# Kernel tuning notes

Measured on AMD Instinct MI355X. Metric: run time of the kernel, lower is better.

## Reference

```python
import math
import jax, jax.numpy as jnp
import numpy as np

B, NH, T, N, D = 4, 8, 2048, 256, 512
THETA = 2 ** 16
LN_EPS = 1e-5
RETRIEVAL_SCALE = 1.0
TWO_PI = 2.0 * math.pi


def _freqs(n):
    # get_freqs: 1/theta**(floor(i/2)*2 / n) / (2*pi)
    i = jnp.arange(n, dtype=jnp.float32)
    q = jnp.floor(i / 2.0) * 2.0
    return 1.0 / (THETA ** (q / n)) / TWO_PI


def _rope(phases, v):
    # phases: [1,1,T,N]; v: [B,nh,T,N]
    ph = (phases % 1.0) * TWO_PI
    pc, ps = jnp.cos(ph), jnp.sin(ph)
    ve, vo = v[..., ::2], v[..., 1::2]
    v_rot = jnp.stack((-vo, ve), axis=-1).reshape(v.shape)  # interleaved rotate
    return v * pc + v_rot * ps


def _l2norm(x):
    return x / jnp.maximum(jnp.linalg.norm(x, axis=-1, keepdims=True), 1e-12)


def setup_inputs() -> dict:
    key = jax.random.key(0)
    ks = jax.random.split(key, 8)
    return {
        "Q": jax.random.normal(ks[0], (B, NH, T, N), jnp.float32),
        "V": jax.random.normal(ks[1], (B, NH, T, D), jnp.float32),
        "x_raw": jax.random.normal(ks[2], (B, T, D), jnp.float32),
        "x_next": jax.random.normal(ks[3], (B, T, D), jnp.float32),
        "theta_Q_w": 0.02 * jax.random.normal(ks[4], (N, D), jnp.float32),
        "theta_K_w": 0.02 * jax.random.normal(ks[5], (N, D), jnp.float32),
        "beta_w": 0.02 * jax.random.normal(ks[6], (NH, D), jnp.float32),
        "memory_gate": jnp.full((1, NH, 1, 1), -2.0, jnp.float32),
        "M0": 0.02 * jax.random.normal(ks[7], (B, NH, N, D), jnp.float32),
    }


def _forward(Q, V, x_raw, x_next, theta_Q_w, theta_K_w, beta_w, memory_gate, M0):
    Bq, nh, Tq, Nq = Q.shape
    # ---- causal RoPE linear attention (K is Q; strictly lower-triangular, no softmax)
    freqs = _freqs(Nq)  # [N]
    phases = jnp.arange(Tq, dtype=jnp.float32)[None, None, :, None] * freqs[None, None, None, :]
    QR = _rope(phases, Q)
    scores = jnp.einsum('bhtn,bhsn->bhts', QR, QR)
    mask = jnp.tril(jnp.ones((Tq, Tq), bool), -1)  # diagonal=-1
    scores = jnp.where(mask, scores, 0.0)
    y_standard = scores @ V  # [B,nh,T,D]

    # ---- memory retrieval (position-invariant query)
    Qm = _l2norm(x_raw @ theta_Q_w.T)  # [B,T,N], shared across heads
    y_memory = jnp.einsum('btn,bhnd->bhtd', Qm, M0)
    mu = y_memory.mean(-1, keepdims=True)
    var = y_memory.var(-1, keepdims=True)  # biased, like torch LayerNorm
    y_memory = (y_memory - mu) * jax.lax.rsqrt(var + LN_EPS) * RETRIEVAL_SCALE

    # ---- delta-rule memory update (detached in the original)
    Km = _l2norm(jax.lax.stop_gradient(x_raw @ theta_K_w.T))         # [B,T,N]
    beta = jax.nn.sigmoid(jax.lax.stop_gradient(x_raw @ beta_w.T))   # [B,T,nh]
    Vm = jax.lax.stop_gradient(x_next)                               # [B,T,D]
    M_init = jax.lax.stop_gradient(M0)

    def step(M, inp):
        k, v, b = inp  # k:[B,N] shared across heads, v:[B,D], b:[B,nh]
        v_old = jnp.einsum('bn,bhnd->bhd', k, M)
        v_new = b[..., None] * v[:, None, :] + (1.0 - b[..., None]) * v_old
        M = M + jnp.einsum('bn,bhd->bhnd', k, v_new - v_old)
        return M, None

    M_new, _ = jax.lax.scan(
        step, M_init,
        (jnp.swapaxes(Km, 0, 1), jnp.swapaxes(Vm, 0, 1), jnp.swapaxes(beta, 0, 1)))

    gate = jax.nn.sigmoid(memory_gate)  # [1,nh,1,1]
    y = (1.0 - gate) * y_standard + gate * y_memory
    return y, M_new


def reference(Q, V, x_raw, x_next, theta_Q_w, theta_K_w, beta_w, memory_gate, M0):
    return _forward(Q, V, x_raw, x_next, theta_Q_w, theta_K_w, beta_w, memory_gate, M0)
```

## Files before the change

kernel.cpp:

```cpp
#include <hip/hip_runtime.h>
#include <hip/hip_bf16.h>
#include <math.h>

#define BBATCH 4
#define NHEAD  8
#define TSEQ   2048
#define NDIM   256
#define DDIM   512

typedef float f32x4 __attribute__((ext_vector_type(4)));
typedef short bf16x8 __attribute__((ext_vector_type(8)));

typedef __attribute__((address_space(3))) unsigned int lds_uint;
typedef __attribute__((address_space(1))) unsigned int g_uint;

__device__ __forceinline__ unsigned short f2bf(float f) {
  __hip_bfloat16 h = __float2bfloat16(f);
  return *reinterpret_cast<unsigned short*>(&h);
}
__device__ __forceinline__ float bf2f(unsigned short u) {
  __hip_bfloat16 h;
  *reinterpret_cast<unsigned short*>(&h) = u;
  return __bfloat162float(h);
}
// ... 235 lines not shown
    int koff = (ks * 32 + khi * 8) * 2;
    bf16x8 ah = *(const bf16x8*)((const char*)Khi + arow * 512 + (koff ^ ((arow & 7) << 4)));
    bf16x8 al = *(const bf16x8*)((const char*)Klo + arow * 512 + (koff ^ ((arow & 7) << 4)));
    bf16x8 bhf[4], blf[4];
#pragma unroll
    for (int si = 0; si < 4; ++si) {
      int brow = si * 16 + l16;
      bhf[si] = *(const bf16x8*)((const char*)Khi + brow * 512 + (koff ^ ((brow & 7) << 4)));
      blf[si] = *(const bf16x8*)((const char*)Klo + brow * 512 + (koff ^ ((brow & 7) << 4)));
    }
#pragma unroll
    for (int si = 0; si < 4; ++si) sacc[si] = mfma16(ah, bhf[si], sacc[si]);
#pragma unroll
    for (int si = 0; si < 4; ++si) sacc[si] = mfma16(ah, blf[si], sacc[si]);
#pragma unroll
    for (int si = 0; si < 4; ++si) sacc[si] = mfma16(al, bhf[si], sacc[si]);
  }
#pragma unroll
  for (int si = 0; si < 4; ++si)
#pragma unroll
    for (int r = 0; r < 4; ++r) {
      int t = wave * 16 + khi * 4 + r, s = si * 16 + l16;
      Bm[t * 64 + s] = (s < t) ? bv[t] * sacc[si][r] : 0.f;
    }
  __syncthreads();
  if (wave == 0) {
    float x[64];
#pragma unroll
    for (int i = 0; i < 64; ++i) x[i] = 0.f;
    long base = (long)blk * 4096;
    const f32x4* BmV = (const f32x4*)Bm;
    float bl = bv[lane];
#pragma unroll
    for (int t = 0; t < 64; ++t) {
      float p0 = 0.f, p1 = 0.f, p2 = 0.f, p3 = 0.f;
#pragma unroll
      for (int rq = 0; rq < 16; ++rq) {
        f32x4 b4 = BmV[t * 16 + rq];
        p0 = fmaf(b4.x, x[rq * 4 + 0], p0);
        p1 = fmaf(b4.y, x[rq * 4 + 1], p1);
        p2 = fmaf(b4.z, x[rq * 4 + 2], p2);
        p3 = fmaf(b4.w, x[rq * 4 + 3], p3);
      }
      float xv = ((lane == t) ? 1.f : 0.f) - ((p0 + p1) + (p2 + p3));
      x[t] = xv;
      float wv = xv * bl;
      unsigned short hi = f2bf(wv);
      Whi[base + t * 64 + lane] = hi;
      Wlo[base + t * 64 + lane] = f2bf(wv - bf2f(hi));
    }
  }
}

__global__ __launch_bounds__(256) void cscan_kernel(
    const unsigned short* __restrict__ Kb,
    const unsigned short* __restrict__ KbT,
    const float* __restrict__ xn,
    const float* __restrict__ M0,
    const unsigned short* __restrict__ Whi,
    const unsigned short* __restrict__ Wlo,
    float* __restrict__ Mout) {
  __shared__ unsigned short Mthi[64 * 256];
  __shared__ unsigned short Mtlo[64 * 256];
  __shared__ unsigned short Kr[64 * 256];
  __shared__ unsigned short Pool[16384];
  __shared__ unsigned short RU0[64 * 64];
  __shared__ unsigned short RU1[64 * 64];
  unsigned short* Wh = Pool;
  unsigned short* Wl = Pool + 4096;
  unsigned short* Krt = Pool;
  int bh = blockIdx.x, dsl = blockIdx.y;
  int b = bh >> 3;
  int d0 = dsl * 64;
  int tid = threadIdx.x, wave = tid >> 6, lane = tid & 63;
  int khi = lane >> 4, l16 = lane & 15;
  const char* KbBase = (const char*)(Kb + (long)b * TSEQ * 256);

  f32x4 macc[4][4];
  const float* M0p = M0 + (long)bh * 256 * 512;
#pragma unroll
  for (int ni = 0; ni < 4; ++ni)
#pragma unroll
    for (int di = 0; di < 4; ++di)
#pragma unroll
      for (int r = 0; r < 4; ++r) {
        int n = wave * 64 + ni * 16 + khi * 4 + r;
        macc[ni][di][r] = M0p[(long)n * 512 + d0 + di * 16 + l16];
      }
#pragma unroll
  for (int ni = 0; ni < 4; ++ni)
#pragma unroll
    for (int di = 0; di < 4; ++di) {
      int n = wave * 64 + ni * 16 + khi * 4;
      int d = di * 16 + l16;
      unsigned short hq[4], lq[4];
#pragma unroll
      for (int r = 0; r < 4; ++r) {
        float v = macc[ni][di][r];
        hq[r] = f2bf(v); lq[r] = f2bf(v - bf2f(hq[r]));
      }
      int off = d * 512 + (((n * 2) ^ ((d & 7) << 4)));
      *(uint2*)((char*)Mthi + off) =
          make_uint2((unsigned)hq[0] | ((unsigned)hq[1] << 16),
                     (unsigned)hq[2] | ((unsigned)hq[3] << 16));
      *(uint2*)((char*)Mtlo + off) =
          make_uint2((unsigned)lq[0] | ((unsigned)lq[1] << 16),
                     (unsigned)lq[2] | ((unsigned)lq[3] << 16));
    }
#pragma unroll
  for (int q = 0; q < 8; ++q) {
    int lin = tid * 16 + q * 4096;
    int t = lin >> 9;
    int c = (lin & 511) ^ KSW(t);
    __builtin_amdgcn_global_load_lds((const g_uint*)(KbBase + (long)t * 512 + c),
                                     (lds_uint*)((char*)Kr + lin), 16, 0, 0);
  }
  __syncthreads();

  for (int ch = 0; ch < 32; ++ch) {
    int tc0 = ch * 64;
    {
      const char* whb = (const char*)(Whi + ((long)bh * 32 + ch) * 4096);
      const char* wlb = (const char*)(Wlo + ((long)bh * 32 + ch) * 4096);
#pragma unroll
      for (int q = 0; q < 2; ++q) {
        int lin = tid * 16 + q * 4096;
        int t = lin >> 7, c = lin & 127;
        int sb = t * 128 + (c ^ ((t & 7) << 4));
        __builtin_amdgcn_global_load_lds((const g_uint*)(whb + sb),
                                         (lds_uint*)((char*)Wh + lin), 16, 0, 0);
        __builtin_amdgcn_global_load_lds((const g_uint*)(wlb + sb),
                                         (lds_uint*)((char*)Wl + lin), 16, 0, 0);
      }
    }
    float vreg[4][4];
    {
      const float* vp = xn + ((long)b * TSEQ + tc0) * 512 + d0;
#pragma unroll
      for (int di = 0; di < 4; ++di)
#pragma unroll
        for (int r = 0; r < 4; ++r) {
          int t = wave * 16 + khi * 4 + r;
          vreg[di][r] = vp[(long)t * 512 + di * 16 + l16];
        }
    }
    __syncthreads();

    f32x4 aacc[4] = {};
#pragma unroll
    for (int ks = 0; ks < 8; ++ks) {
      int arow = wave * 16 + l16;
      int koff = (ks * 32 + khi * 8) * 2;
      bf16x8 af = *(const bf16x8*)((const char*)Kr + arow * 512 + (koff ^ KSW(arow)));
      bf16x8 mh[4], ml[4];
#pragma unroll
      for (int di = 0; di < 4; ++di) {
        int drow = di * 16 + l16;
        mh[di] = *(const bf16x8*)((const char*)Mthi + drow * 512 + (koff ^ ((drow & 7) << 4)));
        ml[di] = *(const bf16x8*)((const char*)Mtlo + drow * 512 + (koff ^ ((drow & 7) << 4)));
      }
#pragma unroll
      for (int di = 0; di < 4; ++di) aacc[di] = mfma16(af, mh[di], aacc[di]);
#pragma unroll
      for (int di = 0; di < 4; ++di) aacc[di] = mfma16(af, ml[di], aacc[di]);
    }
#pragma unroll
    for (int di = 0; di < 4; ++di) {
      int t = wave * 16 + khi * 4;
      int d = di * 16 + l16;
      unsigned short rq[4];
#pragma unroll
      for (int r = 0; r < 4; ++r) rq[r] = f2bf(vreg[di][r] - aacc[di][r]);
      int off = d * 128 + (((t * 2) ^ ((d & 7) << 4)));
      *(uint2*)((char*)RU0 + off) =
          make_uint2((unsigned)rq[0] | ((unsigned)rq[1] << 16),
                     (unsigned)rq[2] | ((unsigned)rq[3] << 16));
    }
    __syncthreads();

    if (ch + 1 < 32) {
      const char* kb2 = KbBase + (long)(tc0 + 64) * 512;
#pragma unroll
      for (int q = 0; q < 8; ++q) {
        int lin = tid * 16 + q * 4096;
        int t = lin >> 9;
        int c = (lin & 511) ^ KSW(t);
        __builtin_amdgcn_global_load_lds((const g_uint*)(kb2 + (long)t * 512 + c),
                                         (lds_uint*)((char*)Kr + lin), 16, 0, 0);
      }
    }

    f32x4 uacc[4] = {};
#pragma unroll
    for (int ks = 0; ks < 2; ++ks) {
      int arow = wave * 16 + l16;
      int soff = (ks * 32 + khi * 8) * 2;
      bf16x8 wh_ = *(const bf16x8*)((const char*)Wh + arow * 128 + (soff ^ ((arow & 7) << 4)));
      bf16x8 wl_ = *(const bf16x8*)((const char*)Wl + arow * 128 + (soff ^ ((arow & 7) << 4)));
      bf16x8 rf[4];
#pragma unroll
      for (int di = 0; di < 4; ++di) {
        int drow = di * 16 + l16;
        rf[di] = *(const bf16x8*)((const char*)RU0 + drow * 128 + (soff ^ ((drow & 7) << 4)));
      }
#pragma unroll
      for (int di = 0; di < 4; ++di) uacc[di] = mfma16(wh_, rf[di], uacc[di]);
#pragma unroll
      for (int di = 0; di < 4; ++di) uacc[di] = mfma16(wl_, rf[di], uacc[di]);
    }
    __syncthreads();

    {
#pragma unroll
      for (int q = 0; q < 8; ++q) {
        int lin = tid * 16 + q * 4096;
        int n = lin >> 7, c = lin & 127;
        long sb = ((long)(b * 256 + n)) * 4096 + (long)tc0 * 2 + (c ^ ((n & 7) << 4));
        __builtin_amdgcn_global_load_lds((const g_uint*)((const char*)KbT + sb),
                                         (lds_uint*)((char*)Krt + lin), 16, 0, 0);
      }
    }
#pragma unroll
    for (int di = 0; di < 4; ++di) {
      int t = wave * 16 + khi * 4;
      int d = di * 16 + l16;
      unsigned short hq[4], lq[4];
#pragma unroll
      for (int r = 0; r < 4; ++r) {
        float u = uacc[di][r];
        hq[r] = f2bf(u); lq[r] = f2bf(u - bf2f(hq[r]));
      }
      int off = d * 128 + (((t * 2) ^ ((d & 7) << 4)));
      *(uint2*)((char*)RU0 + off) =
          make_uint2((unsigned)hq[0] | ((unsigned)hq[1] << 16),
                     (unsigned)hq[2] | ((unsigned)hq[3] << 16));
      *(uint2*)((char*)RU1 + off) =
          make_uint2((unsigned)lq[0] | ((unsigned)lq[1] << 16),
                     (unsigned)lq[2] | ((unsigned)lq[3] << 16));
    }
    __syncthreads();

#pragma unroll
    for (int ks = 0; ks < 2; ++ks) {
      int toff = (ks * 32 + khi * 8) * 2;
      bf16x8 ka[4];
#pragma unroll
      for (int ni = 0; ni < 4; ++ni) {
        int n = wave * 64 + ni * 16 + l16;
        ka[ni] = *(const bf16x8*)((const char*)Krt + n * 128 + (toff ^ ((n & 7) << 4)));
      }
      bf16x8 uh[4], ul[4];
#pragma unroll
      for (int di = 0; di < 4; ++di) {
        int drow = di * 16 + l16;
        uh[di] = *(const bf16x8*)((const char*)RU0 + drow * 128 + (toff ^ ((drow & 7) << 4)));
        ul[di] = *(const bf16x8*)((const char*)RU1 + drow * 128 + (toff ^ ((drow & 7) << 4)));
      }
#pragma unroll
      for (int ni = 0; ni < 4; ++ni)
#pragma unroll
        for (int di = 0; di < 4; ++di)
          macc[ni][di] = mfma16(ka[ni], uh[di], macc[ni][di]);
#pragma unroll
      for (int ni = 0; ni < 4; ++ni)
#pragma unroll
        for (int di = 0; di < 4; ++di)
          macc[ni][di] = mfma16(ka[ni], ul[di], macc[ni][di]);
    }
#pragma unroll
    for (int ni = 0; ni < 4; ++ni)
#pragma unroll
      for (int di = 0; di < 4; ++di) {
        int n = wave * 64 + ni * 16 + khi * 4;
        int d = di * 16 + l16;
        unsigned short hq[4], lq[4];
#pragma unroll
        for (int r = 0; r < 4; ++r) {
          float v = macc[ni][di][r];
          hq[r] = f2bf(v); lq[r] = f2bf(v - bf2f(hq[r]));
        }
        int off = d * 512 + (((n * 2) ^ ((d & 7) << 4)));
        *(uint2*)((char*)Mthi + off) =
            make_uint2((unsigned)hq[0] | ((unsigned)hq[1] << 16),
                       (unsigned)hq[2] | ((unsigned)hq[3] << 16));
        *(uint2*)((char*)Mtlo + off) =
            make_uint2((unsigned)lq[0] | ((unsigned)lq[1] << 16),
                       (unsigned)lq[2] | ((unsigned)lq[3] << 16));
      }
    __syncthreads();
  }

  float* Mo = Mout + (long)bh * 256 * 512;
#pragma unroll
  for (int ni = 0; ni < 4; ++ni)
#pragma unroll
    for (int di = 0; di < 4; ++di)
#pragma unroll
      for (int r = 0; r < 4; ++r) {
        int n = wave * 64 + ni * 16 + khi * 4 + r;
        Mo[(long)n * 512 + d0 + di * 16 + l16] = macc[ni][di][r];
      }
}

__global__ __launch_bounds__(512) void attn_kernel(
    const unsigned short* __restrict__ QR,
    const unsigned short* __restrict__ Vt,
    float* __restrict__ Y) {
  int bh = blockIdx.x;
  int bp = blockIdx.y;
  int wave = threadIdx.x >> 6, lane = threadIdx.x & 63;
  int wr = wave >> 2, wc = wave & 3;
  int khi = lane >> 4, l16 = lane & 15;
  __shared__ unsigned short K_lds[64 * 256];
  __shared__ unsigned short S_lds[128 * 64];
  const unsigned short* QRb = QR + (long)bh * TSEQ * 256;
  const unsigned short* Vtb = Vt + (long)bh * 512 * TSEQ;
  float* yb = Y + (long)bh * TSEQ * 512;
  int lin_base = wave * 4096 + lane * 16;

#pragma unroll 1
  for (int half = 0; half < 2; ++half) {
    int bt = half ? bp : (15 - bp);
    int t0 = bt * 128;
    int nst = 2 * bt + 2;

    bf16x8 qa[8];
    {
      int trow = t0 + wave * 16 + l16;
      const unsigned short* qp = QRb + (long)trow * 256 + khi * 8;
#pragma unroll
      for (int ks = 0; ks < 8; ++ks) qa[ks] = *(const bf16x8*)(qp + ks * 32);
    }
    f32x4 acc[4][8] = {};

#pragma unroll
    for (int q = 0; q < 4; ++q) {
      int linear = lin_base + q * 1024;
      int row = linear >> 9;
      int nc2 = (linear & 511) ^ ((row & 7) << 4);
      __builtin_amdgcn_global_load_lds(
          (const g_uint*)((const char*)QRb + (long)row * 512 + nc2),
          (lds_uint*)((char*)K_lds + (wave * 4 + q) * 1024), 16, 0, 0);
    }
    __syncthreads();

    for (int st = 0; st < nst; ++st) {
      int s0 = st * 64;
      f32x4 sacc[4] = {};
#pragma unroll
      for (int ks = 0; ks < 8; ++ks) {
#pragma unroll
        for (int fc = 0; fc < 4; ++fc) {
          int srow = fc * 16 + l16;
          bf16x8 kf = *(const bf16x8*)(
              (const char*)K_lds + srow * 512 + ((ks * 64 + khi * 16) ^ ((srow & 7) << 4)));
          sacc[fc] = mfma16(qa[ks], kf, sacc[fc]);
        }
      }
#pragma unroll
      for (int fc = 0; fc < 4; ++fc)
#pragma unroll
        for (int r = 0; r < 4; ++r) {
          int srow = wave * 16 + khi * 4 + r;
          int scol = fc * 16 + l16;
          float v = ((s0 + scol) < (t0 + srow)) ? sacc[fc][r] : 0.f;
          *(unsigned short*)(
              (char*)S_lds + srow * 128 + ((scol * 2) ^ ((srow & 7) << 4))) = f2bf(v);
        }
      __syncthreads();

      if (st + 1 < nst) {
        long srow_base = (long)(s0 + 64) * 512;
#pragma unroll
        for (int q = 0; q < 4; ++q) {
          int linear = lin_base + q * 1024;
          int row = linear >> 9;
          int nc2 = (linear & 511) ^ ((row & 7) << 4);
          __builtin_amdgcn_global_load_lds(
              (const g_uint*)((const char*)QRb + srow_base + (long)row * 512 + nc2),
              (lds_uint*)((char*)K_lds + (wave * 4 + q) * 1024), 16, 0, 0);
        }
      }
#pragma unroll
      for (int k2 = 0; k2 < 2; ++k2) {
        bf16x8 af[4];
#pragma unroll
        for (int mi = 0; mi < 4; ++mi) {
          int row = wr * 64 + mi * 16 + l16;
          af[mi] = *(const bf16x8*)(
              (const char*)S_lds + row * 128 + ((k2 * 64 + khi * 16) ^ ((row & 7) << 4)));
        }
#pragma unroll
        for (int nh = 0; nh < 2; ++nh) {
          bf16x8 bfv[4];
#pragma unroll
          for (int nj = 0; nj < 4; ++nj) {
            int d = wc * 128 + (nh * 4 + nj) * 16 + l16;
            bfv[nj] = *(const bf16x8*)(Vtb + (long)d * TSEQ + s0 + k2 * 32 + khi * 8);
          }
#pragma unroll
          for (int mi = 0; mi < 4; ++mi)
#pragma unroll
            for (int nj = 0; nj < 4; ++nj)
              acc[mi][nh * 4 + nj] = mfma16(af[mi], bfv[nj], acc[mi][nh * 4 + nj]);
        }
      }
      __syncthreads();
    }

#pragma unroll
    for (int mi = 0; mi < 4; ++mi)
#pragma unroll
      for (int ni = 0; ni < 8; ++ni)
#pragma unroll
        for (int r = 0; r < 4; ++r) {
          int trow = t0 + wr * 64 + mi * 16 + khi * 4 + r;
          int d = wc * 128 + ni * 16 + l16;
          yb[(long)trow * 512 + d] = acc[mi][ni][r];
        }
  }
}

__global__ __launch_bounds__(512) void combine_kernel(
    const unsigned short* __restrict__ Qm,
    const unsigned short* __restrict__ M0t,
    const float* __restrict__ mg,
    float* __restrict__ Y) {
  int t0 = blockIdx.x * 64;
  int bh = blockIdx.y;
  int b = bh >> 3, h = bh & 7;
  int wv = threadIdx.x >> 6, lane = threadIdx.x & 63;
  int khi = lane >> 4, l16 = lane & 15;
  __shared__ unsigned short A_lds[64 * 256];
  __shared__ float red_s[8][64], red_q[8][64];
  __shared__ float mu_s[64], inv_s[64];
  {
    const unsigned short* src = Qm + ((long)b * TSEQ + t0) * 256;
#pragma unroll
    for (int p = 0; p < 4; ++p) {
      int row = (threadIdx.x >> 5) + p * 16;
      int nc = (threadIdx.x & 31) * 8;
      bf16x8 v = *reinterpret_cast<const bf16x8*>(src + (long)row * 256 + nc);
      *reinterpret_cast<bf16x8*>((char*)A_lds + row * 512 + ((nc * 2) ^ ((row & 7) << 4))) = v;
    }
  }
  __syncthreads();
  f32x4 acc[4][4] = {};
  const unsigned short* Bp = M0t + (long)bh * 512 * 256;
#pragma unroll
  for (int ks = 0; ks < 8; ++ks) {
    bf16x8 a[4], bfr[4];
#pragma unroll
    for (int mi = 0; mi < 4; ++mi) {
      int row = mi * 16 + l16;
      a[mi] = *reinterpret_cast<const bf16x8*>(
          (const char*)A_lds + row * 512 + ((ks * 64 + khi * 16) ^ ((row & 7) << 4)));
    }
#pragma unroll
    for (int ni = 0; ni < 4; ++ni) {
      int d = wv * 64 + ni * 16 + l16;
      bfr[ni] = *reinterpret_cast<const bf16x8*>(Bp + (long)d * 256 + ks * 32 + khi * 8);
    }
#pragma unroll
    for (int mi = 0; mi < 4; ++mi)
#pragma unroll
      for (int ni = 0; ni < 4; ++ni)
        acc[mi][ni] = mfma16(a[mi], bfr[ni], acc[mi][ni]);
  }
  float ps[4][4], pq[4][4];
#pragma unroll
  for (int mi = 0; mi < 4; ++mi)
#pragma unroll
    for (int r = 0; r < 4; ++r) {
      float s = 0.f, q = 0.f;
#pragma unroll
      for (int ni = 0; ni < 4; ++ni) {
        float v = acc[mi][ni][r];
        s += v; q += v * v;
      }
      ps[mi][r] = s; pq[mi][r] = q;
    }
#pragma unroll
  for (int off = 1; off < 16; off <<= 1)
#pragma unroll
    for (int mi = 0; mi < 4; ++mi)
#pragma unroll
      for (int r = 0; r < 4; ++r) {
        ps[mi][r] += __shfl_xor(ps[mi][r], off);
        pq[mi][r] += __shfl_xor(pq[mi][r], off);
      }
  if (l16 == 0) {
#pragma unroll
    for (int mi = 0; mi < 4; ++mi)
#pragma unroll
      for (int r = 0; r < 4; ++r) {
        int row = mi * 16 + khi * 4 + r;
        red_s[wv][row] = ps[mi][r];
        red_q[wv][row] = pq[mi][r];
      }
  }
  __syncthreads();
  if (threadIdx.x < 64) {
    float s = 0.f, q = 0.f;
#pragma unroll
    for (int w2 = 0; w2 < 8; ++w2) { s += red_s[w2][threadIdx.x]; q += red_q[w2][threadIdx.x]; }
    float mu = s / 512.f;
    float var = q / 512.f - mu * mu;
    mu_s[threadIdx.x] = mu;
    inv_s[threadIdx.x] = rsqrtf(var + 1e-5f);
  }
  __syncthreads();
  float gate = 1.f / (1.f + expf(-mg[h]));
  float omg = 1.f - gate;
  float* yb = Y + ((long)bh * TSEQ + t0) * 512;
#pragma unroll
  for (int mi = 0; mi < 4; ++mi)
#pragma unroll
    for (int r = 0; r < 4; ++r) {
      int row = mi * 16 + khi * 4 + r;
      float mu = mu_s[row], inv = inv_s[row];
#pragma unroll
      for (int ni = 0; ni < 4; ++ni) {
        int d = wv * 64 + ni * 16 + l16;
        long off = (long)row * 512 + d;
        float ymv = (acc[mi][ni][r] - mu) * inv;
        yb[off] = omg * yb[off] + gate * ymv;
      }
    }
}

extern "C" void kernel_launch(void* const* d_in, const int* in_sizes, int n_in,
                              void* d_out, int out_size, void* d_ws, size_t ws_size,
                              hipStream_t stream) {
  const float* Q      = (const float*)d_in[0];
  const float* V      = (const float*)d_in[1];
  const float* x_raw  = (const float*)d_in[2];
  const float* x_next = (const float*)d_in[3];
  const float* wq     = (const float*)d_in[4];
  const float* wk     = (const float*)d_in[5];
  const float* bw     = (const float*)d_in[6];
  const float* mg     = (const float*)d_in[7];
  const float* M0     = (const float*)d_in[8];
  float* y = (float*)d_out;
  float* Mout = y + (long)32 * 2048 * 512;

  char* ws = (char*)d_ws;
  unsigned short* QR  = (unsigned short*)(ws);
  unsigned short* Vt  = (unsigned short*)(ws + 33554432);
  unsigned short* M0t = (unsigned short*)(ws + 100663296);
  unsigned short* Qm  = (unsigned short*)(ws + 109051904);
  float*  Km          = (float*)(ws + 113246208);
  float*  beta        = (float*)(ws + 121634816);
  unsigned short* Whi = (unsigned short*)(ws + 33554432);
  unsigned short* Wlo = (unsigned short*)(ws + 41943040);
  unsigned short* Kmb = (unsigned short*)(ws + 50331648);
  unsigned short* KmT = (unsigned short*)(ws + 54525952);

  qkm_kernel<<<dim3(128, 2), dim3(512), 0, stream>>>(x_raw, wq, wk, Qm, Km, Kmb);
  transpose_cast_kernel<<<dim3(4, 32, 4), dim3(256), 0, stream>>>(Km, KmT, 2048, 256);
  beta_kernel<<<dim3(8192), dim3(64), 0, stream>>>(x_raw, bw, beta);
  wprep_kernel<<<dim3(1024), dim3(256), 0, stream>>>(Km, beta, Whi, Wlo);
  cscan_kernel<<<dim3(32, 8), dim3(256), 0, stream>>>(Kmb, KmT, x_next, M0, Whi, Wlo, Mout);
  rope_kernel<<<dim3(32768), dim3(256), 0, stream>>>(Q, QR);
  transpose_cast_kernel<<<dim3(8, 32, 32), dim3(256), 0, stream>>>(V, Vt, 2048, 512);
  transpose_cast_kernel<<<dim3(8, 4, 32), dim3(256), 0, stream>>>(M0, M0t, 256, 512);
  attn_kernel<<<dim3(32, 8), dim3(512), 0, stream>>>(QR, Vt, y);
  combine_kernel<<<dim3(32, 32), dim3(512), 0, stream>>>(Qm, M0t, mg, y);
}
```

Measured before the change: 708.0 us.

## Fuse memory retrieval LayerNorm and gating into attention kernel with 64-row tiles

The separate combine kernel is merged into the attention kernel. The memory retrieval matmul, the LayerNorm and the gated mix are computed in the epilogue, so Y is written once and never read back. The attention tile shrinks from 128 to 64 query rows with a 4x2 wave layout, and the grid doubles to 512 blocks for better load balance across CUs. In exchange, V and M0 tiles are reused over fewer rows, so global and L2 reads of Vt per output row go up.

```diff
diff --git a/kernel.cpp b/kernel.cpp
--- a/kernel.cpp
+++ b/kernel.cpp
@@ -564,64 +564,71 @@
 __global__ __launch_bounds__(512) void attn_kernel(
     const unsigned short* __restrict__ QR,
     const unsigned short* __restrict__ Vt,
+    const unsigned short* __restrict__ Qm,
+    const unsigned short* __restrict__ M0t,
+    const float* __restrict__ mg,
     float* __restrict__ Y) {
   int bh = blockIdx.x;
   int bp = blockIdx.y;
+  int b = bh >> 3, h = bh & 7;
   int wave = threadIdx.x >> 6, lane = threadIdx.x & 63;
-  int wr = wave >> 2, wc = wave & 3;
+  int wr = wave >> 1, wc = wave & 1;
   int khi = lane >> 4, l16 = lane & 15;
   __shared__ unsigned short K_lds[64 * 256];
-  __shared__ unsigned short S_lds[128 * 64];
+  __shared__ unsigned short S_lds[64 * 64];
+  __shared__ float red_s[2][64], red_q[2][64];
   const unsigned short* QRb = QR + (long)bh * TSEQ * 256;
   const unsigned short* Vtb = Vt + (long)bh * 512 * TSEQ;
+  const unsigned short* M0b = M0t + (long)bh * 512 * 256;
   float* yb = Y + (long)bh * TSEQ * 512;
-  int lin_base = wave * 4096 + lane * 16;
+  float gate = 1.f / (1.f + expf(-mg[h]));
+  float omg = 1.f - gate;
+  int lin_base = threadIdx.x * 16;
 
 #pragma unroll 1
   for (int half = 0; half < 2; ++half) {
-    int bt = half ? bp : (15 - bp);
-    int t0 = bt * 128;
-    int nst = 2 * bt + 2;
+    int bt = half ? bp : (31 - bp);
+    int t0 = bt * 64;
+    int nst = bt + 1;
 
     bf16x8 qa[8];
     {
-      int trow = t0 + wave * 16 + l16;
-      const unsigned short* qp = QRb + (long)trow * 256 + khi * 8;
+      const unsigned short* qp = QRb + (long)(t0 + wr * 16 + l16) * 256 + khi * 8;
 #pragma unroll
       for (int ks = 0; ks < 8; ++ks) qa[ks] = *(const bf16x8*)(qp + ks * 32);
     }
-    f32x4 acc[4][8] = {};
+    f32x4 acc[16] = {};
 
 #pragma unroll
     for (int q = 0; q < 4; ++q) {
-      int linear = lin_base + q * 1024;
-      int row = linear >> 9;
-      int nc2 = (linear & 511) ^ ((row & 7) << 4);
+      int lin = lin_base + q * 8192;
+      int row = lin >> 9;
+      int col = (lin & 511) ^ ((row & 7) << 4);
       __builtin_amdgcn_global_load_lds(
-          (const g_uint*)((const char*)QRb + (long)row * 512 + nc2),
-          (lds_uint*)((char*)K_lds + (wave * 4 + q) * 1024), 16, 0, 0);
+          (const g_uint*)((const char*)QRb + (long)row * 512 + col),
+          (lds_uint*)((char*)K_lds + lin), 16, 0, 0);
     }
     __syncthreads();
 
     for (int st = 0; st < nst; ++st) {
       int s0 = st * 64;
-      f32x4 sacc[4] = {};
+      f32x4 sacc[2] = {};
 #pragma unroll
       for (int ks = 0; ks < 8; ++ks) {
 #pragma unroll
-        for (int fc = 0; fc < 4; ++fc) {
-          int srow = fc * 16 + l16;
+        for (int fc = 0; fc < 2; ++fc) {
+          int srow = wc * 32 + fc * 16 + l16;
           bf16x8 kf = *(const bf16x8*)(
               (const char*)K_lds + srow * 512 + ((ks * 64 + khi * 16) ^ ((srow & 7) << 4)));
           sacc[fc] = mfma16(qa[ks], kf, sacc[fc]);
         }
       }
 #pragma unroll
-      for (int fc = 0; fc < 4; ++fc)
+      for (int fc = 0; fc < 2; ++fc)
 #pragma unroll
         for (int r = 0; r < 4; ++r) {
-          int srow = wave * 16 + khi * 4 + r;
-          int scol = fc * 16 + l16;
+          int srow = wr * 16 + khi * 4 + r;
+          int scol = wc * 32 + fc * 16 + l16;
           float v = ((s0 + scol) < (t0 + srow)) ? sacc[fc][r] : 0.f;
           *(unsigned short*)(
               (char*)S_lds + srow * 128 + ((scol * 2) ^ ((srow & 7) << 4))) = f2bf(v);
@@ -632,160 +639,87 @@
         long srow_base = (long)(s0 + 64) * 512;
 #pragma unroll
         for (int q = 0; q < 4; ++q) {
-          int linear = lin_base + q * 1024;
-          int row = linear >> 9;
-          int nc2 = (linear & 511) ^ ((row & 7) << 4);
+          int lin = lin_base + q * 8192;
+          int row = lin >> 9;
+          int col = (lin & 511) ^ ((row & 7) << 4);
           __builtin_amdgcn_global_load_lds(
-              (const g_uint*)((const char*)QRb + srow_base + (long)row * 512 + nc2),
-              (lds_uint*)((char*)K_lds + (wave * 4 + q) * 1024), 16, 0, 0);
+              (const g_uint*)((const char*)QRb + srow_base + (long)row * 512 + col),
+              (lds_uint*)((char*)K_lds + lin), 16, 0, 0);
         }
       }
 #pragma unroll
       for (int k2 = 0; k2 < 2; ++k2) {
-        bf16x8 af[4];
-#pragma unroll
-        for (int mi = 0; mi < 4; ++mi) {
-          int row = wr * 64 + mi * 16 + l16;
-          af[mi] = *(const bf16x8*)(
-              (const char*)S_lds + row * 128 + ((k2 * 64 + khi * 16) ^ ((row & 7) << 4)));
+        int arow = wr * 16 + l16;
+        bf16x8 af = *(const bf16x8*)(
+            (const char*)S_lds + arow * 128 + ((k2 * 64 + khi * 16) ^ ((arow & 7) << 4)));
+#pragma unroll
+        for (int ni = 0; ni < 16; ++ni) {
+          int d = wc * 256 + ni * 16 + l16;
+          bf16x8 bfv = *(const bf16x8*)(Vtb + (long)d * TSEQ + s0 + k2 * 32 + khi * 8);
+          acc[ni] = mfma16(af, bfv, acc[ni]);
         }
-#pragma unroll
-        for (int nh = 0; nh < 2; ++nh) {
-          bf16x8 bfv[4];
-#pragma unroll
-          for (int nj = 0; nj < 4; ++nj) {
-            int d = wc * 128 + (nh * 4 + nj) * 16 + l16;
-            bfv[nj] = *(const bf16x8*)(Vtb + (long)d * TSEQ + s0 + k2 * 32 + khi * 8);
-          }
-#pragma unroll
-          for (int mi = 0; mi < 4; ++mi)
-#pragma unroll
-            for (int nj = 0; nj < 4; ++nj)
-              acc[mi][nh * 4 + nj] = mfma16(af[mi], bfv[nj], acc[mi][nh * 4 + nj]);
+      }
+      __syncthreads();
+    }
+
+    f32x4 ym[16] = {};
+    {
+      const unsigned short* qmp = Qm + ((long)b * TSEQ + t0 + wr * 16 + l16) * 256;
+#pragma unroll
+      for (int ks = 0; ks < 8; ++ks) {
+        bf16x8 a = *(const bf16x8*)(qmp + ks * 32 + khi * 8);
+#pragma unroll
+        for (int ni = 0; ni < 16; ++ni) {
+          int d = wc * 256 + ni * 16 + l16;
+          bf16x8 bm = *(const bf16x8*)(M0b + (long)d * 256 + ks * 32 + khi * 8);
+          ym[ni] = mfma16(a, bm, ym[ni]);
         }
       }
-      __syncthreads();
-    }
-
-#pragma unroll
-    for (int mi = 0; mi < 4; ++mi)
-#pragma unroll
-      for (int ni = 0; ni < 8; ++ni)
-#pragma unroll
-        for (int r = 0; r < 4; ++r) {
-          int trow = t0 + wr * 64 + mi * 16 + khi * 4 + r;
-          int d = wc * 128 + ni * 16 + l16;
-          yb[(long)trow * 512 + d] = acc[mi][ni][r];
-        }
-  }
-}
-
-__global__ __launch_bounds__(512) void combine_kernel(
-    const unsigned short* __restrict__ Qm,
-    const unsigned short* __restrict__ M0t,
-    const float* __restrict__ mg,
-    float* __restrict__ Y) {
-  int t0 = blockIdx.x * 64;
-  int bh = blockIdx.y;
-  int b = bh >> 3, h = bh & 7;
-  int wv = threadIdx.x >> 6, lane = threadIdx.x & 63;
-  int khi = lane >> 4, l16 = lane & 15;
-  __shared__ unsigned short A_lds[64 * 256];
-  __shared__ float red_s[8][64], red_q[8][64];
-  __shared__ float mu_s[64], inv_s[64];
-  {
-    const unsigned short* src = Qm + ((long)b * TSEQ + t0) * 256;
-#pragma unroll
-    for (int p = 0; p < 4; ++p) {
-      int row = (threadIdx.x >> 5) + p * 16;
-      int nc = (threadIdx.x & 31) * 8;
-      bf16x8 v = *reinterpret_cast<const bf16x8*>(src + (long)row * 256 + nc);
-      *reinterpret_cast<bf16x8*>((char*)A_lds + row * 512 + ((nc * 2) ^ ((row & 7) << 4))) = v;
-    }
-  }
-  __syncthreads();
-  f32x4 acc[4][4] = {};
-  const unsigned short* Bp = M0t + (long)bh * 512 * 256;
-#pragma unroll
-  for (int ks = 0; ks < 8; ++ks) {
-    bf16x8 a[4], bfr[4];
-#pragma unroll
-    for (int mi = 0; mi < 4; ++mi) {
-      int row = mi * 16 + l16;
-      a[mi] = *reinterpret_cast<const bf16x8*>(
-          (const char*)A_lds + row * 512 + ((ks * 64 + khi * 16) ^ ((row & 7) << 4)));
-    }
-#pragma unroll
-    for (int ni = 0; ni < 4; ++ni) {
-      int d = wv * 64 + ni * 16 + l16;
-      bfr[ni] = *reinterpret_cast<const bf16x8*>(Bp + (long)d * 256 + ks * 32 + khi * 8);
-    }
-#pragma unroll
-    for (int mi = 0; mi < 4; ++mi)
-#pragma unroll
-      for (int ni = 0; ni < 4; ++ni)
-        acc[mi][ni] = mfma16(a[mi], bfr[ni], acc[mi][ni]);
-  }
-  float ps[4][4], pq[4][4];
-#pragma unroll
-  for (int mi = 0; mi < 4; ++mi)
+    }
+    float ps[4], pq[4];
 #pragma unroll
     for (int r = 0; r < 4; ++r) {
       float s = 0.f, q = 0.f;
 #pragma unroll
-      for (int ni = 0; ni < 4; ++ni) {
-        float v = acc[mi][ni][r];
-        s += v; q += v * v;
-      }
-      ps[mi][r] = s; pq[mi][r] = q;
-    }
-#pragma unroll
-  for (int off = 1; off < 16; off <<= 1)
-#pragma unroll
-    for (int mi = 0; mi < 4; ++mi)
+      for (int ni = 0; ni < 16; ++ni) { float v = ym[ni][r]; s += v; q += v * v; }
+      ps[r] = s; pq[r] = q;
+    }
+#pragma unroll
+    for (int off = 1; off < 16; off <<= 1)
 #pragma unroll
       for (int r = 0; r < 4; ++r) {
-        ps[mi][r] += __shfl_xor(ps[mi][r], off);
-        pq[mi][r] += __shfl_xor(pq[mi][r], off);
-      }
-  if (l16 == 0) {
-#pragma unroll
-    for (int mi = 0; mi < 4; ++mi)
+        ps[r] += __shfl_xor(ps[r], off);
+        pq[r] += __shfl_xor(pq[r], off);
+      }
+    if (l16 == 0) {
 #pragma unroll
       for (int r = 0; r < 4; ++r) {
-        int row = mi * 16 + khi * 4 + r;
-        red_s[wv][row] = ps[mi][r];
-        red_q[wv][row] = pq[mi][r];
-      }
-  }
-  __syncthreads();
-  if (threadIdx.x < 64) {
-    float s = 0.f, q = 0.f;
-#pragma unroll
-    for (int w2 = 0; w2 < 8; ++w2) { s += red_s[w2][threadIdx.x]; q += red_q[w2][threadIdx.x]; }
-    float mu = s / 512.f;
-    float var = q / 512.f - mu * mu;
-    mu_s[threadIdx.x] = mu;
-    inv_s[threadIdx.x] = rsqrtf(var + 1e-5f);
-  }
-  __syncthreads();
-  float gate = 1.f / (1.f + expf(-mg[h]));
-  float omg = 1.f - gate;
-  float* yb = Y + ((long)bh * TSEQ + t0) * 512;
-#pragma unroll
-  for (int mi = 0; mi < 4; ++mi)
+        int row = wr * 16 + khi * 4 + r;
+        red_s[wc][row] = ps[r];
+        red_q[wc][row] = pq[r];
+      }
+    }
+    __syncthreads();
+    float mu[4], inv[4];
 #pragma unroll
     for (int r = 0; r < 4; ++r) {
-      int row = mi * 16 + khi * 4 + r;
-      float mu = mu_s[row], inv = inv_s[row];
-#pragma unroll
-      for (int ni = 0; ni < 4; ++ni) {
-        int d = wv * 64 + ni * 16 + l16;
-        long off = (long)row * 512 + d;
-        float ymv = (acc[mi][ni][r] - mu) * inv;
-        yb[off] = omg * yb[off] + gate * ymv;
-      }
-    }
+      int row = wr * 16 + khi * 4 + r;
+      float s = red_s[0][row] + red_s[1][row];
+      float q = red_q[0][row] + red_q[1][row];
+      float m_ = s / 512.f;
+      mu[r] = m_;
+      inv[r] = rsqrtf(q / 512.f - m_ * m_ + 1e-5f);
+    }
+#pragma unroll
+    for (int ni = 0; ni < 16; ++ni)
+#pragma unroll
+      for (int r = 0; r < 4; ++r) {
+        int trow = t0 + wr * 16 + khi * 4 + r;
+        int d = wc * 256 + ni * 16 + l16;
+        float ymn = (ym[ni][r] - mu[r]) * inv[r];
+        yb[(long)trow * 512 + d] = omg * acc[ni][r] + gate * ymn;
+      }
+  }
 }
 
 extern "C" void kernel_launch(void* const* d_in, const int* in_sizes, int n_in,
@@ -823,6 +757,5 @@
   rope_kernel<<<dim3(32768), dim3(256), 0, stream>>>(Q, QR);
   transpose_cast_kernel<<<dim3(8, 32, 32), dim3(256), 0, stream>>>(V, Vt, 2048, 512);
   transpose_cast_kernel<<<dim3(8, 4, 32), dim3(256), 0, stream>>>(M0, M0t, 256, 512);
-  attn_kernel<<<dim3(32, 8), dim3(512), 0, stream>>>(QR, Vt, y);
-  combine_kernel<<<dim3(32, 32), dim3(512), 0, stream>>>(Qm, M0t, mg, y);
-}
+  attn_kernel<<<dim3(32, 16), dim3(512), 0, stream>>>(QR, Vt, Qm, M0t, mg, y);
+}
```

Result: slower. 1.673 ms (+136.4%).

## Fuse memory retrieval and LayerNorm combine into attention kernel epilogue

Applied to the files above, without the earlier changes.

Moves the Qm·M0 retrieval GEMM, its LayerNorm and the gated combine into attn_kernel, so combine_kernel is removed. The attention output is no longer written to Y and then read back; each tile computes y_memory up front, holds it as packed bf16 in registers, and writes the blended result once. This removes one launch and a full read-modify-write pass over the 128MB fp32 output. In exchange it adds register pressure (under a new launch_bounds(512,2) request), rounds y_memory to bf16 before the blend, and adds extra M0t/Qm global loads per tile.

```diff
diff --git a/kernel.cpp b/kernel.cpp
--- a/kernel.cpp
+++ b/kernel.cpp
@@ -561,20 +561,28 @@
       }
 }
 
-__global__ __launch_bounds__(512) void attn_kernel(
+__global__ __launch_bounds__(512, 2) void attn_kernel(
     const unsigned short* __restrict__ QR,
     const unsigned short* __restrict__ Vt,
+    const unsigned short* __restrict__ Qm,
+    const unsigned short* __restrict__ M0t,
+    const float* __restrict__ mg,
     float* __restrict__ Y) {
   int bh = blockIdx.x;
   int bp = blockIdx.y;
+  int b = bh >> 3, h = bh & 7;
   int wave = threadIdx.x >> 6, lane = threadIdx.x & 63;
   int wr = wave >> 2, wc = wave & 3;
   int khi = lane >> 4, l16 = lane & 15;
   __shared__ unsigned short K_lds[64 * 256];
   __shared__ unsigned short S_lds[128 * 64];
+  __shared__ float red_s[4][128], red_q[4][128];
   const unsigned short* QRb = QR + (long)bh * TSEQ * 256;
   const unsigned short* Vtb = Vt + (long)bh * 512 * TSEQ;
+  const unsigned short* M0b = M0t + (long)bh * 512 * 256;
   float* yb = Y + (long)bh * TSEQ * 512;
+  float gate = 1.f / (1.f + expf(-mg[h]));
+  float omg = 1.f - gate;
   int lin_base = wave * 4096 + lane * 16;
 
 #pragma unroll 1
@@ -582,6 +590,83 @@
     int bt = half ? bp : (15 - bp);
     int t0 = bt * 128;
     int nst = 2 * bt + 2;
+
+    unsigned int ymp[4][8][2];
+    {
+      f32x4 ym[4][8] = {};
+#pragma unroll
+      for (int ks = 0; ks < 8; ++ks) {
+        bf16x8 a[4], bm[8];
+#pragma unroll
+        for (int mi = 0; mi < 4; ++mi) {
+          long row = (long)b * TSEQ + t0 + wr * 64 + mi * 16 + l16;
+          a[mi] = *(const bf16x8*)(Qm + row * 256 + ks * 32 + khi * 8);
+        }
+#pragma unroll
+        for (int ni = 0; ni < 8; ++ni) {
+          int d = wc * 128 + ni * 16 + l16;
+          bm[ni] = *(const bf16x8*)(M0b + (long)d * 256 + ks * 32 + khi * 8);
+        }
+#pragma unroll
+        for (int mi = 0; mi < 4; ++mi)
+#pragma unroll
+          for (int ni = 0; ni < 8; ++ni)
+            ym[mi][ni] = mfma16(a[mi], bm[ni], ym[mi][ni]);
+      }
+      float ps[4][4], pq[4][4];
+#pragma unroll
+      for (int mi = 0; mi < 4; ++mi)
+#pragma unroll
+        for (int r = 0; r < 4; ++r) {
+          float s = 0.f, q = 0.f;
+#pragma unroll
+          for (int ni = 0; ni < 8; ++ni) { float v = ym[mi][ni][r]; s += v; q += v * v; }
+          ps[mi][r] = s; pq[mi][r] = q;
+        }
+#pragma unroll
+      for (int off = 1; off < 16; off <<= 1)
+#pragma unroll
+        for (int mi = 0; mi < 4; ++mi)
+#pragma unroll
+          for (int r = 0; r < 4; ++r) {
+            ps[mi][r] += __shfl_xor(ps[mi][r], off);
+            pq[mi][r] += __shfl_xor(pq[mi][r], off);
+          }
+      if (l16 == 0) {
+#pragma unroll
+        for (int mi = 0; mi < 4; ++mi)
+#pragma unroll
+          for (int r = 0; r < 4; ++r) {
+            int row = wr * 64 + mi * 16 + khi * 4 + r;
+            red_s[wc][row] = ps[mi][r];
+            red_q[wc][row] = pq[mi][r];
+          }
+      }
+      __syncthreads();
+#pragma unroll
+      for (int mi = 0; mi < 4; ++mi) {
+        float mu[4], inv[4];
+#pragma unroll
+        for (int r = 0; r < 4; ++r) {
+          int row = wr * 64 + mi * 16 + khi * 4 + r;
+          float s = red_s[0][row] + red_s[1][row] + red_s[2][row] + red_s[3][row];
+          float q = red_q[0][row] + red_q[1][row] + red_q[2][row] + red_q[3][row];
+          float m_ = s / 512.f;
+          mu[r] = m_;
+          inv[r] = rsqrtf(q / 512.f - m_ * m_ + 1e-5f);
+        }
+#pragma unroll
+        for (int ni = 0; ni < 8; ++ni) {
+          unsigned short n0 = f2bf((ym[mi][ni][0] - mu[0]) * inv[0]);
+          unsigned short n1 = f2bf((ym[mi][ni][1] - mu[1]) * inv[1]);
+          unsigned short n2 = f2bf((ym[mi][ni][2] - mu[2]) * inv[2]);
+          unsigned short n3 = f2bf((ym[mi][ni][3] - mu[3]) * inv[3]);
+          ymp[mi][ni][0] = (unsigned)n0 | ((unsigned)n1 << 16);
+          ymp[mi][ni][1] = (unsigned)n2 | ((unsigned)n3 << 16);
+        }
+      }
+      __syncthreads();
+    }
 
     bf16x8 qa[8];
     {
@@ -670,122 +755,20 @@
 #pragma unroll
     for (int mi = 0; mi < 4; ++mi)
 #pragma unroll
-      for (int ni = 0; ni < 8; ++ni)
-#pragma unroll
-        for (int r = 0; r < 4; ++r) {
-          int trow = t0 + wr * 64 + mi * 16 + khi * 4 + r;
-          int d = wc * 128 + ni * 16 + l16;
-          yb[(long)trow * 512 + d] = acc[mi][ni][r];
-        }
-  }
-}
-
-__global__ __launch_bounds__(512) void combine_kernel(
-    const unsigned short* __restrict__ Qm,
-    const unsigned short* __restrict__ M0t,
-    const float* __restrict__ mg,
-    float* __restrict__ Y) {
-  int t0 = blockIdx.x * 64;
-  int bh = blockIdx.y;
-  int b = bh >> 3, h = bh & 7;
-  int wv = threadIdx.x >> 6, lane = threadIdx.x & 63;
-  int khi = lane >> 4, l16 = lane & 15;
-  __shared__ unsigned short A_lds[64 * 256];
-  __shared__ float red_s[8][64], red_q[8][64];
-  __shared__ float mu_s[64], inv_s[64];
-  {
-    const unsigned short* src = Qm + ((long)b * TSEQ + t0) * 256;
-#pragma unroll
-    for (int p = 0; p < 4; ++p) {
-      int row = (threadIdx.x >> 5) + p * 16;
-      int nc = (threadIdx.x & 31) * 8;
-      bf16x8 v = *reinterpret_cast<const bf16x8*>(src + (long)row * 256 + nc);
-      *reinterpret_cast<bf16x8*>((char*)A_lds + row * 512 + ((nc * 2) ^ ((row & 7) << 4))) = v;
-    }
-  }
-  __syncthreads();
-  f32x4 acc[4][4] = {};
-  const unsigned short* Bp = M0t + (long)bh * 512 * 256;
-#pragma unroll
-  for (int ks = 0; ks < 8; ++ks) {
-    bf16x8 a[4], bfr[4];
-#pragma unroll
-    for (int mi = 0; mi < 4; ++mi) {
-      int row = mi * 16 + l16;
-      a[mi] = *reinterpret_cast<const bf16x8*>(
-          (const char*)A_lds + row * 512 + ((ks * 64 + khi * 16) ^ ((row & 7) << 4)));
-    }
-#pragma unroll
-    for (int ni = 0; ni < 4; ++ni) {
-      int d = wv * 64 + ni * 16 + l16;
-      bfr[ni] = *reinterpret_cast<const bf16x8*>(Bp + (long)d * 256 + ks * 32 + khi * 8);
-    }
-#pragma unroll
-    for (int mi = 0; mi < 4; ++mi)
-#pragma unroll
-      for (int ni = 0; ni < 4; ++ni)
-        acc[mi][ni] = mfma16(a[mi], bfr[ni], acc[mi][ni]);
-  }
-  float ps[4][4], pq[4][4];
-#pragma unroll
-  for (int mi = 0; mi < 4; ++mi)
-#pragma unroll
-    for (int r = 0; r < 4; ++r) {
-      float s = 0.f, q = 0.f;
-#pragma unroll
-      for (int ni = 0; ni < 4; ++ni) {
-        float v = acc[mi][ni][r];
-        s += v; q += v * v;
-      }
-      ps[mi][r] = s; pq[mi][r] = q;
-    }
-#pragma unroll
-  for (int off = 1; off < 16; off <<= 1)
-#pragma unroll
-    for (int mi = 0; mi < 4; ++mi)
-#pragma unroll
-      for (int r = 0; r < 4; ++r) {
-        ps[mi][r] += __shfl_xor(ps[mi][r], off);
-        pq[mi][r] += __shfl_xor(pq[mi][r], off);
-      }
-  if (l16 == 0) {
-#pragma unroll
-    for (int mi = 0; mi < 4; ++mi)
-#pragma unroll
-      for (int r = 0; r < 4; ++r) {
-        int row = mi * 16 + khi * 4 + r;
-        red_s[wv][row] = ps[mi][r];
-        red_q[wv][row] = pq[mi][r];
-      }
-  }
-  __syncthreads();
-  if (threadIdx.x < 64) {
-    float s = 0.f, q = 0.f;
-#pragma unroll
-    for (int w2 = 0; w2 < 8; ++w2) { s += red_s[w2][threadIdx.x]; q += red_q[w2][threadIdx.x]; }
-    float mu = s / 512.f;
-    float var = q / 512.f - mu * mu;
-    mu_s[threadIdx.x] = mu;
-    inv_s[threadIdx.x] = rsqrtf(var + 1e-5f);
-  }
-  __syncthreads();
-  float gate = 1.f / (1.f + expf(-mg[h]));
-  float omg = 1.f - gate;
-  float* yb = Y + ((long)bh * TSEQ + t0) * 512;
-#pragma unroll
-  for (int mi = 0; mi < 4; ++mi)
-#pragma unroll
-    for (int r = 0; r < 4; ++r) {
-      int row = mi * 16 + khi * 4 + r;
-      float mu = mu_s[row], inv = inv_s[row];
-#pragma unroll
-      for (int ni = 0; ni < 4; ++ni) {
-        int d = wv * 64 + ni * 16 + l16;
-        long off = (long)row * 512 + d;
-        float ymv = (acc[mi][ni][r] - mu) * inv;
-        yb[off] = omg * yb[off] + gate * ymv;
-      }
-    }
+      for (int ni = 0; ni < 8; ++ni) {
+        unsigned int u0 = ymp[mi][ni][0], u1 = ymp[mi][ni][1];
+        float y0 = bf2f((unsigned short)(u0 & 0xffff));
+        float y1 = bf2f((unsigned short)(u0 >> 16));
+        float y2 = bf2f((unsigned short)(u1 & 0xffff));
+        float y3 = bf2f((unsigned short)(u1 >> 16));
+        int d = wc * 128 + ni * 16 + l16;
+        long base = (long)(t0 + wr * 64 + mi * 16 + khi * 4) * 512 + d;
+        yb[base + 0 * 512] = omg * acc[mi][ni][0] + gate * y0;
+        yb[base + 1 * 512] = omg * acc[mi][ni][1] + gate * y1;
+        yb[base + 2 * 512] = omg * acc[mi][ni][2] + gate * y2;
+        yb[base + 3 * 512] = omg * acc[mi][ni][3] + gate * y3;
+      }
+  }
 }
 
 extern "C" void kernel_launch(void* const* d_in, const int* in_sizes, int n_in,
@@ -823,6 +806,5 @@
   rope_kernel<<<dim3(32768), dim3(256), 0, stream>>>(Q, QR);
   transpose_cast_kernel<<<dim3(8, 32, 32), dim3(256), 0, stream>>>(V, Vt, 2048, 512);
   transpose_cast_kernel<<<dim3(8, 4, 32), dim3(256), 0, stream>>>(M0, M0t, 256, 512);
-  attn_kernel<<<dim3(32, 8), dim3(512), 0, stream>>>(QR, Vt, y);
-  combine_kernel<<<dim3(32, 32), dim3(512), 0, stream>>>(Qm, M0t, mg, y);
-}
+  attn_kernel<<<dim3(32, 8), dim3(512), 0, stream>>>(QR, Vt, Qm, M0t, mg, y);
+}
```

Measured after the change: 910.6 us. +28.6%, slower.

## Halve attention query tile to 64 rows and double grid for occupancy

Applied to the files above, without the earlier changes.

The causal attention kernel now processes 64-row query tiles instead of 128, and pairs tile bt with 31-bt so each block gets balanced work. The grid doubles to 512 blocks, and waves are rearranged as 4x2, with each wave owning 16 rows by 256 output columns. Launch bounds request 4 blocks per CU, which caps registers per thread. This gives more parallelism and finer causal skipping, at the cost of less reuse of V loads per block and doubling the S computation relative to the output work.

```diff
diff --git a/kernel.cpp b/kernel.cpp
--- a/kernel.cpp
+++ b/kernel.cpp
@@ -561,67 +561,66 @@
       }
 }
 
-__global__ __launch_bounds__(512) void attn_kernel(
+__global__ __launch_bounds__(512, 4) void attn_kernel(
     const unsigned short* __restrict__ QR,
     const unsigned short* __restrict__ Vt,
     float* __restrict__ Y) {
   int bh = blockIdx.x;
   int bp = blockIdx.y;
   int wave = threadIdx.x >> 6, lane = threadIdx.x & 63;
-  int wr = wave >> 2, wc = wave & 3;
+  int wr = wave >> 1, wc = wave & 1;
   int khi = lane >> 4, l16 = lane & 15;
   __shared__ unsigned short K_lds[64 * 256];
-  __shared__ unsigned short S_lds[128 * 64];
+  __shared__ unsigned short S_lds[64 * 64];
   const unsigned short* QRb = QR + (long)bh * TSEQ * 256;
   const unsigned short* Vtb = Vt + (long)bh * 512 * TSEQ;
   float* yb = Y + (long)bh * TSEQ * 512;
-  int lin_base = wave * 4096 + lane * 16;
+  int lin_base = threadIdx.x * 16;
 
 #pragma unroll 1
   for (int half = 0; half < 2; ++half) {
-    int bt = half ? bp : (15 - bp);
-    int t0 = bt * 128;
-    int nst = 2 * bt + 2;
+    int bt = half ? bp : (31 - bp);
+    int t0 = bt * 64;
+    int nst = bt + 1;
 
     bf16x8 qa[8];
     {
-      int trow = t0 + wave * 16 + l16;
-      const unsigned short* qp = QRb + (long)trow * 256 + khi * 8;
+      const unsigned short* qp = QRb + (long)(t0 + wr * 16 + l16) * 256 + khi * 8;
 #pragma unroll
       for (int ks = 0; ks < 8; ++ks) qa[ks] = *(const bf16x8*)(qp + ks * 32);
     }
-    f32x4 acc[4][8] = {};
+    f32x4 acc[16] = {};
 
 #pragma unroll
     for (int q = 0; q < 4; ++q) {
-      int linear = lin_base + q * 1024;
-      int row = linear >> 9;
-      int nc2 = (linear & 511) ^ ((row & 7) << 4);
+      int lin = lin_base + q * 8192;
+      int row = lin >> 9;
+      int col = (lin & 511) ^ ((row & 7) << 4);
       __builtin_amdgcn_global_load_lds(
-          (const g_uint*)((const char*)QRb + (long)row * 512 + nc2),
-          (lds_uint*)((char*)K_lds + (wave * 4 + q) * 1024), 16, 0, 0);
+          (const g_uint*)((const char*)QRb + (long)row * 512 + col),
+          (lds_uint*)((char*)K_lds + lin), 16, 0, 0);
     }
     __syncthreads();
 
     for (int st = 0; st < nst; ++st) {
       int s0 = st * 64;
-      f32x4 sacc[4] = {};
+      f32x4 sacc[2] = {};
 #pragma unroll
       for (int ks = 0; ks < 8; ++ks) {
 #pragma unroll
-        for (int fc = 0; fc < 4; ++fc) {
-          int srow = fc * 16 + l16;
+        for (int fc = 0; fc < 2; ++fc) {
+          int srow = wc * 32 + fc * 16 + l16;
           bf16x8 kf = *(const bf16x8*)(
               (const char*)K_lds + srow * 512 + ((ks * 64 + khi * 16) ^ ((srow & 7) << 4)));
           sacc[fc] = mfma16(qa[ks], kf, sacc[fc]);
         }
       }
 #pragma unroll
-      for (int fc = 0; fc < 4; ++fc)
+      for (int fc = 0; fc < 2; ++fc)
 #pragma unroll
         for (int r = 0; r < 4; ++r) {
-          int srow = wave * 16 + khi * 4 + r;
-          int scol = fc * 16 + l16;
+          int srow = wr * 16 + khi * 4 + r;
+          int scol = wc * 32 + fc * 16 + l16;
           float v = ((s0 + scol) < (t0 + srow)) ? sacc[fc][r] : 0.f;
           *(unsigned short*)(
               (char*)S_lds + srow * 128 + ((scol * 2) ^ ((srow & 7) << 4))) = f2bf(v);
@@ -632,51 +631,37 @@
         long srow_base = (long)(s0 + 64) * 512;
 #pragma unroll
         for (int q = 0; q < 4; ++q) {
-          int linear = lin_base + q * 1024;
-          int row = linear >> 9;
-          int nc2 = (linear & 511) ^ ((row & 7) << 4);
+          int lin = lin_base + q * 8192;
+          int row = lin >> 9;
+          int col = (lin & 511) ^ ((row & 7) << 4);
           __builtin_amdgcn_global_load_lds(
-              (const g_uint*)((const char*)QRb + srow_base + (long)row * 512 + nc2),
-              (lds_uint*)((char*)K_lds + (wave * 4 + q) * 1024), 16, 0, 0);
+              (const g_uint*)((const char*)QRb + srow_base + (long)row * 512 + col),
+              (lds_uint*)((char*)K_lds + lin), 16, 0, 0);
         }
       }
 #pragma unroll
       for (int k2 = 0; k2 < 2; ++k2) {
-        bf16x8 af[4];
-#pragma unroll
-        for (int mi = 0; mi < 4; ++mi) {
-          int row = wr * 64 + mi * 16 + l16;
-          af[mi] = *(const bf16x8*)(
-              (const char*)S_lds + row * 128 + ((k2 * 64 + khi * 16) ^ ((row & 7) << 4)));
+        int arow = wr * 16 + l16;
+        bf16x8 af = *(const bf16x8*)(
+            (const char*)S_lds + arow * 128 + ((k2 * 64 + khi * 16) ^ ((arow & 7) << 4)));
+#pragma unroll
+        for (int ni = 0; ni < 16; ++ni) {
+          int d = wc * 256 + ni * 16 + l16;
+          bf16x8 bfv = *(const bf16x8*)(Vtb + (long)d * TSEQ + s0 + k2 * 32 + khi * 8);
+          acc[ni] = mfma16(af, bfv, acc[ni]);
         }
-#pragma unroll
-        for (int nh = 0; nh < 2; ++nh) {
-          bf16x8 bfv[4];
-#pragma unroll
-          for (int nj = 0; nj < 4; ++nj) {
-            int d = wc * 128 + (nh * 4 + nj) * 16 + l16;
-            bfv[nj] = *(const bf16x8*)(Vtb + (long)d * TSEQ + s0 + k2 * 32 + khi * 8);
-          }
-#pragma unroll
-          for (int mi = 0; mi < 4; ++mi)
-#pragma unroll
-            for (int nj = 0; nj < 4; ++nj)
-              acc[mi][nh * 4 + nj] = mfma16(af[mi], bfv[nj], acc[mi][nh * 4 + nj]);
-        }
       }
       __syncthreads();
     }
 
 #pragma unroll
-    for (int mi = 0; mi < 4; ++mi)
-#pragma unroll
-      for (int ni = 0; ni < 8; ++ni)
-#pragma unroll
-        for (int r = 0; r < 4; ++r) {
-          int trow = t0 + wr * 64 + mi * 16 + khi * 4 + r;
-          int d = wc * 128 + ni * 16 + l16;
-          yb[(long)trow * 512 + d] = acc[mi][ni][r];
-        }
+    for (int ni = 0; ni < 16; ++ni)
+#pragma unroll
+      for (int r = 0; r < 4; ++r) {
+        int trow = t0 + wr * 16 + khi * 4 + r;
+        int d = wc * 256 + ni * 16 + l16;
+        yb[(long)trow * 512 + d] = acc[ni][r];
+      }
   }
 }
 
@@ -823,6 +808,6 @@
   rope_kernel<<<dim3(32768), dim3(256), 0, stream>>>(Q, QR);
   transpose_cast_kernel<<<dim3(8, 32, 32), dim3(256), 0, stream>>>(V, Vt, 2048, 512);
   transpose_cast_kernel<<<dim3(8, 4, 32), dim3(256), 0, stream>>>(M0, M0t, 256, 512);
-  attn_kernel<<<dim3(32, 8), dim3(512), 0, stream>>>(QR, Vt, y);
+  attn_kernel<<<dim3(32, 16), dim3(512), 0, stream>>>(QR, Vt, y);
   combine_kernel<<<dim3(32, 32), dim3(512), 0, stream>>>(Qm, M0t, mg, y);
 }
```

After: 1.247 ms. 1.76x slower.
